# Kernel tuning notes

Measured on AMD Instinct MI355X. Metric: run time of the kernel, lower is better.

Reference implementation:

```python
import math
import jax, jax.numpy as jnp
import numpy as np

NH = 16          # num_attention_heads
MAX_REL = 512    # max_relative_positions


def _t4(x):
    # [B, N, H] -> [B, NH, N, H/NH]  (transpose_for_scores)
    B, N, H = x.shape
    return x.reshape(B, N, NH, -1).transpose(0, 2, 1, 3)


def setup_inputs() -> dict:
    key = jax.random.key(0)
    ks = jax.random.split(key, 6)
    B, N, H = 1, 2048, 1024
    hidden_states = jax.random.normal(ks[0], (B, N, H), jnp.float32)
    attention_mask = jnp.ones((B, 1, N, N), jnp.int32)
    ids = jnp.arange(N, dtype=jnp.int32)
    relative_pos = ids[:, None] - ids[None, :]              # [N, N], build_relative_position
    rel_embeddings = jax.random.normal(ks[1], (2 * MAX_REL, H), jnp.float32) * 0.02
    in_proj_w = jax.random.normal(ks[2], (3 * H, H), jnp.float32) * 0.02
    q_bias = jnp.zeros((H,), jnp.float32)
    v_bias = jnp.zeros((H,), jnp.float32)
    pos_proj_w = jax.random.normal(ks[3], (H, H), jnp.float32) * 0.02
    pos_q_proj_w = jax.random.normal(ks[4], (H, H), jnp.float32) * 0.02
    pos_q_proj_b = jnp.zeros((H,), jnp.float32)
    return dict(hidden_states=hidden_states, attention_mask=attention_mask,
                relative_pos=relative_pos, rel_embeddings=rel_embeddings,
                in_proj_w=in_proj_w, q_bias=q_bias, v_bias=v_bias,
                pos_proj_w=pos_proj_w, pos_q_proj_w=pos_q_proj_w,
                pos_q_proj_b=pos_q_proj_b)


def reference(hidden_states, attention_mask, relative_pos, rel_embeddings,
              in_proj_w, q_bias, v_bias, pos_proj_w, pos_q_proj_w, pos_q_proj_b):
    B, N, H = hidden_states.shape
    dh = H // NH
    scale_factor = 1 + 2  # 1 + len(["c2p", "p2c"])
    scale = math.sqrt(dh * scale_factor)

    # fused QKV projection; chunk(3, dim=-1) AFTER transpose_for_scores -> per-head q|k|v layout
    qp = hidden_states @ in_proj_w.T                          # [B, N, 3H]
    q, k, v = jnp.split(_t4(qp), 3, axis=-1)                  # each [B, NH, N, dh]
    q = q + _t4(q_bias[None, None, :])
    v = v + _t4(v_bias[None, None, :])
    q = q / scale

    scores = jnp.einsum('bhqd,bhkd->bhqk', q, k)              # content-content

    # disentangled relative-position bias
    span = min(N, MAX_REL)                                    # att_span
    rel = rel_embeddings[MAX_REL - span:MAX_REL + span][None] # [1, 2S, H]
    rpos = relative_pos.astype(jnp.int32)[None, None]         # [1, 1, N, N]

    # c2p: content-to-position
    pos_k = _t4(rel @ pos_proj_w.T)                           # [1, NH, 2S, dh]
    c2p = jnp.einsum('bhqd,xhsd->bhqs', q, pos_k)             # [B, NH, N, 2S]
    c2p_pos = jnp.clip(rpos + span, 0, 2 * span - 1)
    c2p = jnp.take_along_axis(c2p, c2p_pos, axis=-1)          # gather -> [B, NH, N, N]

    # p2c: position-to-content
    pos_q = _t4(rel @ pos_q_proj_w.T + pos_q_proj_b) / scale  # [1, NH, 2S, dh]
    p2c = jnp.einsum('bhkd,xhsd->bhks', k, pos_q)             # [B, NH, N, 2S]
    p2c_pos = jnp.clip(-rpos + span, 0, 2 * span - 1)
    p2c = jnp.take_along_axis(p2c, p2c_pos, axis=-1)          # [B, NH, K, Q]
    p2c = jnp.swapaxes(p2c, -1, -2)                           # -> [B, NH, Q, K]

    scores = scores + c2p + p2c

    # XSoftmax: masked softmax, masked probs zeroed
    m = attention_mask.astype(bool)                           # [B, 1, N, N]
    probs = jax.nn.softmax(jnp.where(m, scores, -jnp.inf), axis=-1)
    probs = jnp.where(m, probs, 0.0)

    ctx = jnp.einsum('bhqk,bhkd->bhqd', probs, v)             # [B, NH, N, dh]
    return ctx.transpose(0, 2, 1, 3).reshape(B, N, H)
```

## Files before the change

### kernel.cpp

```cpp
#include <hip/hip_runtime.h>
#include <hip/hip_bf16.h>

typedef __bf16 bf16;
typedef __attribute__((ext_vector_type(8))) __bf16 bf16x8;
typedef __attribute__((ext_vector_type(8))) float f32x8;
typedef __attribute__((ext_vector_type(4))) float f32x4;

#define MFMA(a,b,c) __builtin_amdgcn_mfma_f32_16x16x32_bf16((a),(b),(c),0,0,0)

__device__ __forceinline__ bf16x8 ld8(const bf16* p){ bf16x8 v; __builtin_memcpy(&v,p,16); return v; }
__device__ __forceinline__ void   st8(bf16* p, bf16x8 v){ __builtin_memcpy(p,&v,16); }
__device__ __forceinline__ bf16x8 ld8f(const float* p) {
    f32x8 v; __builtin_memcpy(&v, p, 32);
    bf16x8 r;
    #pragma unroll
    for (int i = 0; i < 8; i++) r[i] = (bf16)v[i];
    return r;
}

__global__ __launch_bounds__(256)
void gemm_all(const float* __restrict__ X, const float* __restrict__ Win,
              const float* __restrict__ REL, const float* __restrict__ Wpk,
              const float* __restrict__ Wpq,
              const float* __restrict__ qb, const float* __restrict__ vb,
              bf16* __restrict__ Qw, bf16* __restrict__ Kw, bf16* __restrict__ Vtw,
              float* __restrict__ part)
{
    __shared__ __attribute__((aligned(16))) bf16 As[128][32];
    __shared__ __attribute__((aligned(16))) bf16 Bs[128][32];

    const int tid = threadIdx.x, w = tid >> 6, lane = tid & 63;
    const int l15 = lane & 15, quad = lane >> 4;
    const int wr = w >> 1, wc = w & 1;

    const int bid = blockIdx.x;
    int mode, m0, n0, kbeg, kend, arr = 0, z = 0;
    const float *A, *B;
    const int K = 1024;
    if (bid < 384) {
        mode = 0; A = X; B = Win;
        n0 = (bid % 24) * 128; m0 = (bid / 24) * 128;
        kbeg = 0; kend = 1024;
    } else {
        mode = 1; A = REL;
        int t = bid - 384;
        int x = t & 7, y = (t >> 3) & 15; z = t >> 7;
        arr = y >> 3;
        B = arr ? Wpq : Wpk;
        n0 = x * 128; m0 = (y & 7) * 128;
        kbeg = z * 256; kend = kbeg + 256;
    }
    const int srow = tid >> 2, scol = (tid & 3) * 8;

    f32x4 acc[4][4] = {};
    for (int k0 = kbeg; k0 < kend; k0 += 32) {
        __syncthreads();
        st8(&As[srow][scol],    ld8f(A + (size_t)(m0 + srow) * K + k0 + scol));
        st8(&As[srow+64][scol], ld8f(A + (size_t)(m0 + 64 + srow) * K + k0 + scol));
        st8(&Bs[srow][scol],    ld8f(B + (size_t)(n0 + srow) * K + k0 + scol));
        st8(&Bs[srow+64][scol], ld8f(B + (size_t)(n0 + 64 + srow) * K + k0 + scol));
        __syncthreads();
        bf16x8 a[4], b[4];
        #pragma unroll
        for (int i = 0; i < 4; i++) a[i] = ld8(&As[wr*64 + i*16 + l15][quad*8]);
        #pragma unroll
        for (int j = 0; j < 4; j++) b[j] = ld8(&Bs[wc*64 + j*16 + l15][quad*8]);
        #pragma unroll
        for (int i = 0; i < 4; i++)
            #pragma unroll
            for (int j = 0; j < 4; j++)
                acc[i][j] = MFMA(a[i], b[j], acc[i][j]);
    }

    const float inv_scale = 0.07216878364870323f;
    #pragma unroll
    for (int i = 0; i < 4; i++) {
        #pragma unroll
        for (int j = 0; j < 4; j++) {
            #pragma unroll
            for (int r = 0; r < 4; r++) {
                int row = m0 + wr*64 + i*16 + quad*4 + r;
                int col = n0 + wc*64 + j*16 + l15;
                float v = acc[i][j][r];
                if (mode == 0) {
                    int h = col / 192, rr = col % 192;
                    if (rr < 64)
                        Qw[((size_t)h*2048 + row)*64 + rr] =
                            (bf16)((v + qb[h*64 + rr]) * inv_scale);
                    else if (rr < 128)
                        Kw[((size_t)h*2048 + row)*64 + (rr - 64)] = (bf16)v;
                    else
                        Vtw[((size_t)h*64 + (rr - 128))*2048 + row] =
                            (bf16)(v + vb[h*64 + (rr - 128)]);
                } else {
                    part[(((size_t)(arr*4 + z)*1024 + row)*1024) + col] = v;
                }
            }
        }
    }
}

__global__ __launch_bounds__(256)
void pos_merge(const float* __restrict__ part, const float* __restrict__ pqb,
               bf16* __restrict__ PKw, bf16* __restrict__ PQw)
{
    int e = blockIdx.x * 256 + threadIdx.x;
    int arr = e >> 20, r = (e >> 10) & 1023, c = e & 1023;
    const float* p = part + ((size_t)arr*4) * 1048576 + (size_t)r * 1024 + c;
    float v = p[0] + p[1048576] + p[2*1048576] + p[3*1048576];
    int h = c >> 6, d = c & 63;
    if (arr == 0) PKw[((size_t)h*1024 + r)*64 + d] = (bf16)v;
    else          PQw[((size_t)h*1024 + r)*64 + d] =
                      (bf16)((v + pqb[c]) * 0.07216878364870323f);
}

__global__ __launch_bounds__(256)
void band_gemm(const bf16* __restrict__ Qw, const bf16* __restrict__ Kw,
               const bf16* __restrict__ PKw, const bf16* __restrict__ PQw,
               bf16* __restrict__ C2Pw, bf16* __restrict__ P2Cw)
{
    const int tid = threadIdx.x, w = tid >> 6, lane = tid & 63;
    const int l15 = lane & 15, quad = lane >> 4;
    const int wr = w >> 1, wc = w & 1;

    const int bid  = blockIdx.x;
    const int mat  = bid >> 11;
    const int rest = bid & 2047;
    const int h    = rest >> 7;
    const int t    = rest & 127;
    const int m0 = (t >> 3) * 128, n0 = (t & 7) * 128;

    const bf16* A = (mat ? Kw  : Qw)  + (size_t)h * 2048 * 64;
    const bf16* B = (mat ? PQw : PKw) + (size_t)h * 1024 * 64;
    bf16*       C = (mat ? P2Cw : C2Pw) + (size_t)h * 2048 * 1024;

    f32x4 acc[4][4] = {};
    #pragma unroll
    for (int s = 0; s < 2; s++) {
        bf16x8 a[4], b[4];
        #pragma unroll
        for (int i = 0; i < 4; i++)
            a[i] = ld8(A + (size_t)(m0 + wr*64 + i*16 + l15)*64 + s*32 + quad*8);
        #pragma unroll
        for (int j = 0; j < 4; j++)
            b[j] = ld8(B + (size_t)(n0 + wc*64 + j*16 + l15)*64 + s*32 + quad*8);
        #pragma unroll
        for (int i = 0; i < 4; i++)
            #pragma unroll
            for (int j = 0; j < 4; j++)
                acc[i][j] = MFMA(a[i], b[j], acc[i][j]);
    }
    #pragma unroll
    for (int i = 0; i < 4; i++)
        #pragma unroll
        for (int j = 0; j < 4; j++)
            #pragma unroll
            for (int r = 0; r < 4; r++)
                C[(size_t)(m0 + wr*64 + i*16 + quad*4 + r)*1024
                  + n0 + wc*64 + j*16 + l15] = (bf16)acc[i][j][r];
}

__global__ __launch_bounds__(64, 2)
void attn_kernel(const bf16* __restrict__ Q, const bf16* __restrict__ Kc,
                 const bf16* __restrict__ Vt,
                 const bf16* __restrict__ C2P, const bf16* __restrict__ P2C,
                 float* __restrict__ Opart, float* __restrict__ Lpart)
{
    __shared__ __attribute__((aligned(16))) bf16 Ps[16][72];

    const int lane = threadIdx.x;
    const int l15 = lane & 15, quad = lane >> 4;
    const int h = blockIdx.y, qw0 = blockIdx.x * 16;
    const int split = blockIdx.z;

    const bf16* Qh   = Q   + (size_t)h * 2048 * 64;
    const bf16* Kh   = Kc  + (size_t)h * 2048 * 64;
    const bf16* Vh   = Vt  + (size_t)h * 64 * 2048;
    const bf16* C2Ph = C2P + (size_t)h * 2048 * 1024;
    const bf16* P2Ch = P2C + (size_t)h * 2048 * 1024;

    bf16x8 qa[2];
    #pragma unroll
    for (int s = 0; s < 2; s++)
        qa[s] = ld8(Qh + (size_t)(qw0 + l15)*64 + s*32 + quad*8);

    f32x4 oacc[4] = {};
    float psum[4] = {0.f, 0.f, 0.f, 0.f};

    for (int kb = split; kb < 32; kb += 2) {
        const int k0 = kb * 64;

        bf16x8 kf[4][2];
        #pragma unroll
        for (int nt = 0; nt < 4; nt++)
            #pragma unroll
            for (int s = 0; s < 2; s++)
                kf[nt][s] = ld8(Kh + (size_t)(k0 + nt*16 + l15)*64 + s*32 + quad*8);

        f32x4 sacc[4] = {};
        #pragma unroll
        for (int s = 0; s < 2; s++)
            #pragma unroll
            for (int nt = 0; nt < 4; nt++)
                sacc[nt] = MFMA(qa[s], kf[nt][s], sacc[nt]);

        const int dbase = qw0 - k0 + 512;
        float val[4][4];
        if (dbase <= -15 || dbase >= 1086) {
            const int e = (dbase <= -15) ? 0 : 1023;
            float ce[4], pe[4];
            #pragma unroll
            for (int r = 0; r < 4; r++)
                ce[r] = (float)C2Ph[(size_t)(qw0 + quad*4 + r)*1024 + e];
            #pragma unroll
            for (int nt = 0; nt < 4; nt++)
                pe[nt] = (float)P2Ch[(size_t)(k0 + nt*16 + l15)*1024 + e];
            #pragma unroll
            for (int nt = 0; nt < 4; nt++)
                #pragma unroll
                for (int r = 0; r < 4; r++)
                    val[nt][r] = sacc[nt][r] + ce[r] + pe[nt];
        } else {
            #pragma unroll
            for (int nt = 0; nt < 4; nt++)
                #pragma unroll
                for (int r = 0; r < 4; r++) {
                    int d = dbase + quad*4 + r - (nt*16 + l15);
                    d = min(max(d, 0), 1023);
                    val[nt][r] = sacc[nt][r]
                        + (float)C2Ph[(size_t)(qw0 + quad*4 + r)*1024 + d]
                        + (float)P2Ch[(size_t)(k0 + nt*16 + l15)*1024 + d];
                }
        }

        #pragma unroll
        for (int nt = 0; nt < 4; nt++)
            #pragma unroll
            for (int r = 0; r < 4; r++) {
                float e = __expf(val[nt][r]);
                psum[r] += e;
                Ps[quad*4 + r][nt*16 + l15] = (bf16)e;
            }

        #pragma unroll
        for (int s = 0; s < 2; s++) {
            bf16x8 pa = ld8(&Ps[l15][s*32 + quad*8]);
            #pragma unroll
            for (int dt = 0; dt < 4; dt++) {
                bf16x8 vf = ld8(Vh + (size_t)(dt*16 + l15)*2048 + k0 + s*32 + quad*8);
                oacc[dt] = MFMA(pa, vf, oacc[dt]);
            }
        }
    }

    #pragma unroll
    for (int r = 0; r < 4; r++)
        #pragma unroll
        for (int m = 1; m < 16; m <<= 1)
            psum[r] += __shfl_xor(psum[r], m);

    const size_t pb = (size_t)((split << 4) + h);
    #pragma unroll
    for (int dt = 0; dt < 4; dt++)
        #pragma unroll
        for (int r = 0; r < 4; r++) {
            int row = qw0 + quad*4 + r;
            Opart[(pb*2048 + row)*64 + dt*16 + l15] = oacc[dt][r];
        }
    if (l15 == 0)
        #pragma unroll
        for (int r = 0; r < 4; r++)
            Lpart[pb*2048 + qw0 + quad*4 + r] = psum[r];
}

__global__ __launch_bounds__(256)
void attn_merge(const float* __restrict__ Opart, const float* __restrict__ Lpart,
                float* __restrict__ out)
{
    int e = blockIdx.x * 256 + threadIdx.x;
    int row = e >> 10, c = e & 1023;
    int h = c >> 6, d = c & 63;
    float o = Opart[((size_t)h*2048 + row)*64 + d]
            + Opart[(((size_t)16 + h)*2048 + row)*64 + d];
    float l = Lpart[(size_t)h*2048 + row] + Lpart[((size_t)16 + h)*2048 + row];
    out[e] = o / l;
}

extern "C" void kernel_launch(void* const* d_in, const int* in_sizes, int n_in,
                              void* d_out, int out_size, void* d_ws, size_t ws_size,
                              hipStream_t stream)
{
    (void)in_sizes; (void)n_in; (void)out_size; (void)ws_size;
    const float* X   = (const float*)d_in[0];
    const float* REL = (const float*)d_in[3];
    const float* Win = (const float*)d_in[4];
    const float* qb  = (const float*)d_in[5];
    const float* vb  = (const float*)d_in[6];
    const float* Wpk = (const float*)d_in[7];
    const float* Wpq = (const float*)d_in[8];
    const float* pqb = (const float*)d_in[9];
    float* out = (float*)d_out;

    char* ws = (char*)d_ws;
    const size_t MB = 1024u * 1024u;
    bf16*  Qw    = (bf16*)(ws);
    bf16*  Kw    = (bf16*)(ws + 4*MB);
    bf16*  Vtw   = (bf16*)(ws + 8*MB);
    bf16*  PKw   = (bf16*)(ws + 12*MB);
    bf16*  PQw   = (bf16*)(ws + 14*MB);
    float* Ppart = (float*)(ws + 16*MB);
    bf16*  C2Pw  = (bf16*)(ws + 16*MB);
    bf16*  P2Cw  = (bf16*)(ws + 80*MB);
    float* Opart = (float*)(ws + 144*MB);
    float* Lpart = (float*)(ws + 160*MB);

    gemm_all<<<dim3(896), 256, 0, stream>>>(X, Win, REL, Wpk, Wpq, qb, vb,
                                            Qw, Kw, Vtw, Ppart);
    pos_merge<<<dim3(8192), 256, 0, stream>>>(Ppart, pqb, PKw, PQw);
    band_gemm<<<dim3(4096), 256, 0, stream>>>(Qw, Kw, PKw, PQw, C2Pw, P2Cw);
    attn_kernel<<<dim3(128, 16, 2), 64, 0, stream>>>(Qw, Kw, Vtw, C2Pw, P2Cw,
                                                     Opart, Lpart);
    attn_merge<<<dim3(8192), 256, 0, stream>>>(Opart, Lpart, out);
}
```

Before: 387.4 us.

## Drop split-K for position projections and widen attention split with two-wave blocks

The position-projection GEMM no longer splits K four ways with a separate merge kernel. Each tile now runs the full K loop and writes PK/PQ in bf16 directly, which removes the fp32 partial buffer traffic and one launch. The attention kernel packs two 16-row waves per block and splits the key range four ways instead of two, with the merge summing four partials. The aim is more parallelism and occupancy in the attention stage, at the cost of fewer, longer GEMM blocks and extra partial-output traffic.

```diff
diff --git a/kernel.cpp b/kernel.cpp
--- a/kernel.cpp
+++ b/kernel.cpp
@@ -23,8 +23,9 @@
               const float* __restrict__ REL, const float* __restrict__ Wpk,
               const float* __restrict__ Wpq,
               const float* __restrict__ qb, const float* __restrict__ vb,
+              const float* __restrict__ pqb,
               bf16* __restrict__ Qw, bf16* __restrict__ Kw, bf16* __restrict__ Vtw,
-              float* __restrict__ part)
+              bf16* __restrict__ PKw, bf16* __restrict__ PQw)
 {
     __shared__ __attribute__((aligned(16))) bf16 As[128][32];
     __shared__ __attribute__((aligned(16))) bf16 Bs[128][32];
@@ -34,26 +35,23 @@
     const int wr = w >> 1, wc = w & 1;
 
     const int bid = blockIdx.x;
-    int mode, m0, n0, kbeg, kend, arr = 0, z = 0;
+    int mode, m0, n0, arr = 0;
     const float *A, *B;
     const int K = 1024;
     if (bid < 384) {
         mode = 0; A = X; B = Win;
         n0 = (bid % 24) * 128; m0 = (bid / 24) * 128;
-        kbeg = 0; kend = 1024;
     } else {
         mode = 1; A = REL;
         int t = bid - 384;
-        int x = t & 7, y = (t >> 3) & 15; z = t >> 7;
-        arr = y >> 3;
+        arr = t >> 6; t &= 63;
         B = arr ? Wpq : Wpk;
-        n0 = x * 128; m0 = (y & 7) * 128;
-        kbeg = z * 256; kend = kbeg + 256;
+        m0 = (t >> 3) * 128; n0 = (t & 7) * 128;
     }
     const int srow = tid >> 2, scol = (tid & 3) * 8;
 
     f32x4 acc[4][4] = {};
-    for (int k0 = kbeg; k0 < kend; k0 += 32) {
+    for (int k0 = 0; k0 < K; k0 += 32) {
         __syncthreads();
         st8(&As[srow][scol],    ld8f(A + (size_t)(m0 + srow) * K + k0 + scol));
         st8(&As[srow+64][scol], ld8f(A + (size_t)(m0 + 64 + srow) * K + k0 + scol));
@@ -93,25 +91,16 @@
                         Vtw[((size_t)h*64 + (rr - 128))*2048 + row] =
                             (bf16)(v + vb[h*64 + (rr - 128)]);
                 } else {
-                    part[(((size_t)(arr*4 + z)*1024 + row)*1024) + col] = v;
+                    int h = col >> 6, d = col & 63;
+                    if (arr == 0)
+                        PKw[((size_t)h*1024 + row)*64 + d] = (bf16)v;
+                    else
+                        PQw[((size_t)h*1024 + row)*64 + d] =
+                            (bf16)((v + pqb[col]) * inv_scale);
                 }
             }
         }
     }
-}
-
-__global__ __launch_bounds__(256)
-void pos_merge(const float* __restrict__ part, const float* __restrict__ pqb,
-               bf16* __restrict__ PKw, bf16* __restrict__ PQw)
-{
-    int e = blockIdx.x * 256 + threadIdx.x;
-    int arr = e >> 20, r = (e >> 10) & 1023, c = e & 1023;
-    const float* p = part + ((size_t)arr*4) * 1048576 + (size_t)r * 1024 + c;
-    float v = p[0] + p[1048576] + p[2*1048576] + p[3*1048576];
-    int h = c >> 6, d = c & 63;
-    if (arr == 0) PKw[((size_t)h*1024 + r)*64 + d] = (bf16)v;
-    else          PQw[((size_t)h*1024 + r)*64 + d] =
-                      (bf16)((v + pqb[c]) * 0.07216878364870323f);
 }
 
 __global__ __launch_bounds__(256)
@@ -160,17 +149,18 @@
                   + n0 + wc*64 + j*16 + l15] = (bf16)acc[i][j][r];
 }
 
-__global__ __launch_bounds__(64, 2)
+__global__ __launch_bounds__(128, 8)
 void attn_kernel(const bf16* __restrict__ Q, const bf16* __restrict__ Kc,
                  const bf16* __restrict__ Vt,
                  const bf16* __restrict__ C2P, const bf16* __restrict__ P2C,
                  float* __restrict__ Opart, float* __restrict__ Lpart)
 {
-    __shared__ __attribute__((aligned(16))) bf16 Ps[16][72];
-
-    const int lane = threadIdx.x;
+    __shared__ __attribute__((aligned(16))) bf16 Ps[2][16][72];
+
+    const int wv   = threadIdx.x >> 6;
+    const int lane = threadIdx.x & 63;
     const int l15 = lane & 15, quad = lane >> 4;
-    const int h = blockIdx.y, qw0 = blockIdx.x * 16;
+    const int h = blockIdx.y, qw0 = (blockIdx.x * 2 + wv) * 16;
     const int split = blockIdx.z;
 
     const bf16* Qh   = Q   + (size_t)h * 2048 * 64;
@@ -187,7 +177,7 @@
     f32x4 oacc[4] = {};
     float psum[4] = {0.f, 0.f, 0.f, 0.f};
 
-    for (int kb = split; kb < 32; kb += 2) {
+    for (int kb = split; kb < 32; kb += 4) {
         const int k0 = kb * 64;
 
         bf16x8 kf[4][2];
@@ -239,12 +229,12 @@
             for (int r = 0; r < 4; r++) {
                 float e = __expf(val[nt][r]);
                 psum[r] += e;
-                Ps[quad*4 + r][nt*16 + l15] = (bf16)e;
+                Ps[wv][quad*4 + r][nt*16 + l15] = (bf16)e;
             }
 
         #pragma unroll
         for (int s = 0; s < 2; s++) {
-            bf16x8 pa = ld8(&Ps[l15][s*32 + quad*8]);
+            bf16x8 pa = ld8(&Ps[wv][l15][s*32 + quad*8]);
             #pragma unroll
             for (int dt = 0; dt < 4; dt++) {
                 bf16x8 vf = ld8(Vh + (size_t)(dt*16 + l15)*2048 + k0 + s*32 + quad*8);
@@ -280,9 +270,13 @@
     int e = blockIdx.x * 256 + threadIdx.x;
     int row = e >> 10, c = e & 1023;
     int h = c >> 6, d = c & 63;
-    float o = Opart[((size_t)h*2048 + row)*64 + d]
-            + Opart[(((size_t)16 + h)*2048 + row)*64 + d];
-    float l = Lpart[(size_t)h*2048 + row] + Lpart[((size_t)16 + h)*2048 + row];
+    float o = 0.f, l = 0.f;
+    #pragma unroll
+    for (int z = 0; z < 4; z++) {
+        size_t pb = (size_t)(z*16 + h);
+        o += Opart[(pb*2048 + row)*64 + d];
+        l += Lpart[pb*2048 + row];
+    }
     out[e] = o / l;
 }
 
@@ -308,17 +302,15 @@
     bf16*  Vtw   = (bf16*)(ws + 8*MB);
     bf16*  PKw   = (bf16*)(ws + 12*MB);
     bf16*  PQw   = (bf16*)(ws + 14*MB);
-    float* Ppart = (float*)(ws + 16*MB);
     bf16*  C2Pw  = (bf16*)(ws + 16*MB);
     bf16*  P2Cw  = (bf16*)(ws + 80*MB);
     float* Opart = (float*)(ws + 144*MB);
-    float* Lpart = (float*)(ws + 160*MB);
-
-    gemm_all<<<dim3(896), 256, 0, stream>>>(X, Win, REL, Wpk, Wpq, qb, vb,
-                                            Qw, Kw, Vtw, Ppart);
-    pos_merge<<<dim3(8192), 256, 0, stream>>>(Ppart, pqb, PKw, PQw);
+    float* Lpart = (float*)(ws + 176*MB);
+
+    gemm_all<<<dim3(512), 256, 0, stream>>>(X, Win, REL, Wpk, Wpq, qb, vb, pqb,
+                                            Qw, Kw, Vtw, PKw, PQw);
     band_gemm<<<dim3(4096), 256, 0, stream>>>(Qw, Kw, PKw, PQw, C2Pw, P2Cw);
-    attn_kernel<<<dim3(128, 16, 2), 64, 0, stream>>>(Qw, Kw, Vtw, C2Pw, P2Cw,
+    attn_kernel<<<dim3(64, 16, 4), 128, 0, stream>>>(Qw, Kw, Vtw, C2Pw, P2Cw,
                                                      Opart, Lpart);
     attn_merge<<<dim3(8192), 256, 0, stream>>>(Opart, Lpart, out);
 }
```

New measurement: 521.7 us. 1.35x slower.
